# Kernel tuning notes

Hardware: AMD Instinct MI355X
Metric: run time of the kernel (lower is better)

Reference implementation:

```python
import jax, jax.numpy as jnp
import numpy as np
import math

B, S, D, H, FF = 8, 1024, 1024, 16, 4096
DH = D // H
EPS = 1e-5


def _layernorm(x, g, b):
    mu = jnp.mean(x, axis=-1, keepdims=True)
    var = jnp.mean((x - mu) ** 2, axis=-1, keepdims=True)
    return (x - mu) * jax.lax.rsqrt(var + EPS) * g + b


def _gelu_tanh(x):
    c = math.sqrt(2.0 / math.pi)
    return 0.5 * x * (1.0 + jnp.tanh(c * (x + 0.044715 * x ** 3)))


def setup_inputs() -> dict:
    key = jax.random.key(0)
    ks = jax.random.split(key, 8)
    s = lambda d: 1.0 / math.sqrt(d)
    return {
        "x": jax.random.normal(ks[0], (B, S, D), jnp.float32),
        "ln1_g": jnp.ones((D,), jnp.float32),
        "ln1_b": jnp.zeros((D,), jnp.float32),
        "w_qkv": jax.random.normal(ks[1], (3 * D, D), jnp.float32) * s(D),
        "b_qkv": jax.random.normal(ks[2], (3 * D,), jnp.float32) * 0.02,
        "w_o": jax.random.normal(ks[3], (D, D), jnp.float32) * s(D),
        "b_o": jax.random.normal(ks[4], (D,), jnp.float32) * 0.02,
        "ln2_g": jnp.ones((D,), jnp.float32),
        "ln2_b": jnp.zeros((D,), jnp.float32),
        "w1": jax.random.normal(ks[5], (FF, D), jnp.float32) * s(D),
        "b1": jax.random.normal(ks[6], (FF,), jnp.float32) * 0.02,
        "w2": jax.random.normal(ks[7], (D, FF), jnp.float32) * s(FF),
        "b2": jnp.zeros((D,), jnp.float32),
    }


def reference(x, ln1_g, ln1_b, w_qkv, b_qkv, w_o, b_o, ln2_g, ln2_b, w1, b1, w2, b2):
    # --- pre-LN causal self-attention ---
    h = _layernorm(x, ln1_g, ln1_b)
    qkv = h @ w_qkv.T + b_qkv                      # [B,S,3D]
    q, k, v = jnp.split(qkv, 3, axis=-1)
    q = q.reshape(B, S, H, DH)
    k = k.reshape(B, S, H, DH)
    v = v.reshape(B, S, H, DH)
    scores = jnp.einsum("bqhd,bkhd->bhqk", q, k) / math.sqrt(DH)
    causal = jnp.triu(jnp.ones((S, S), jnp.bool_), 1)  # True above diagonal
    scores = jnp.where(causal, -jnp.inf, scores)
    attn = jax.nn.softmax(scores, axis=-1)
    o = jnp.einsum("bhqk,bkhd->bqhd", attn, v).reshape(B, S, D)
    x = x + (o @ w_o.T + b_o)
    # --- FFN ---
    h = _layernorm(x, ln2_g, ln2_b)
    h = _gelu_tanh(h @ w1.T + b1) @ w2.T + b2
    return x + h
```

## Files before the change

### kernel.cpp

```cpp
#include <hip/hip_runtime.h>
#include <math.h>


typedef __bf16 bf16_t;
typedef __bf16 bf16x4 __attribute__((ext_vector_type(4)));
typedef __bf16 bf16x8 __attribute__((ext_vector_type(8)));
typedef float f32x4 __attribute__((ext_vector_type(4)));

__device__ __forceinline__ void async16(const void* g, void* l) {
    __builtin_amdgcn_global_load_lds(
        (const __attribute__((address_space(1))) void*)g,
        (__attribute__((address_space(3))) void*)l,
        16, 0, 0);
}

__global__ __launch_bounds__(256) void f2b_all(
    const float* __restrict__ s0, const float* __restrict__ s1,
    const float* __restrict__ s2, const float* __restrict__ s3,
    bf16_t* __restrict__ d0, bf16_t* __restrict__ d1,
    bf16_t* __restrict__ d2, bf16_t* __restrict__ d3) {
    const int g = blockIdx.x * 256 + threadIdx.x;
    const float* s;
    bf16_t* d;
    int off;
    if (g < 786432)       { s = s0; d = d0; off = g; }
    else if (g < 1048576) { s = s1; d = d1; off = g - 786432; }
    else if (g < 2097152) { s = s2; d = d2; off = g - 1048576; }
    else                  { s = s3; d = d3; off = g - 2097152; }
    const int i = off * 4;
    const float4 v = *(const float4*)(s + i);
    bf16x4 o;
    o[0] = (bf16_t)v.x; o[1] = (bf16_t)v.y; o[2] = (bf16_t)v.z; o[3] = (bf16_t)v.w;
    *(bf16x4*)(d + i) = o;
}

__global__ __launch_bounds__(256) void ln_bf16(const float* __restrict__ x,
                                               const float* __restrict__ g,
                                               const float* __restrict__ bb,
                                               bf16_t* __restrict__ out) {
    const int tid = threadIdx.x;
    const int row = blockIdx.x;
    const float4 xv = *(const float4*)(x + row * 1024 + tid * 4);
    float s1 = xv.x + xv.y + xv.z + xv.w;
    float s2 = xv.x * xv.x + xv.y * xv.y + xv.z * xv.z + xv.w * xv.w;
#pragma unroll
    for (int m = 32; m >= 1; m >>= 1) {
        s1 += __shfl_xor(s1, m);
        s2 += __shfl_xor(s2, m);
    }
    __shared__ float r1[4], r2[4];
    const int wid = tid >> 6, lane = tid & 63;
    if (lane == 0) { r1[wid] = s1; r2[wid] = s2; }
    __syncthreads();
    s1 = r1[0] + r1[1] + r1[2] + r1[3];
    s2 = r2[0] + r2[1] + r2[2] + r2[3];
    const float mu = s1 * (1.0f / 1024.0f);
    const float var = s2 * (1.0f / 1024.0f) - mu * mu;
    const float rs = rsqrtf(var + 1e-5f);
    const float4 gv = *(const float4*)(g + tid * 4);
    const float4 bv = *(const float4*)(bb + tid * 4);
    bf16x4 o;
    o[0] = (bf16_t)((xv.x - mu) * rs * gv.x + bv.x);
    o[1] = (bf16_t)((xv.y - mu) * rs * gv.y + bv.y);
    o[2] = (bf16_t)((xv.z - mu) * rs * gv.z + bv.z);
    o[3] = (bf16_t)((xv.w - mu) * rs * gv.w + bv.w);
    *(bf16x4*)(out + row * 1024 + tid * 4) = o;
}

template <int MODE>
__global__ __launch_bounds__(256, 2) void gemm_bt(
    const bf16_t* __restrict__ A, const bf16_t* __restrict__ W,
    const float* __restrict__ bias, const float* __restrict__ resid,
    bf16_t* __restrict__ outb, float* __restrict__ outf,
    bf16_t* __restrict__ vt, int N, int K) {
    __shared__ bf16_t As[128 * 64];
    __shared__ bf16_t Bs[128 * 64];
    const int tid = threadIdx.x;
    const int w = tid >> 6;
    const int lane = tid & 63;
    const int l15 = lane & 15;
    const int quad = lane >> 4;

    const int nbn = N >> 7;
    const int per = 8 * nbn;
    const int lid = blockIdx.x;
    const int bm = (lid / per) * 8 + (lid % per) % 8;
    const int bn = (lid % per) / 8;
    const int m0 = bm * 128;
    const int n0 = bn * 128;
    const int wm = (w & 1) * 64;
    const int wn = (w >> 1) * 64;

    int rr[4], so[4];
#pragma unroll
    for (int q = 0; q < 4; q++) {
        const int c = q * 256 + w * 64 + lane;
        rr[q] = c >> 3;
        so[q] = ((c & 7) ^ (rr[q] & 7)) * 8;
    }
    const bf16_t* pA[4];
    const bf16_t* pB[4];
#pragma unroll
    for (int q = 0; q < 4; q++) {
        pA[q] = A + (size_t)(m0 + rr[q]) * K + so[q];
        pB[q] = W + (size_t)(n0 + rr[q]) * K + so[q];
    }

    f32x4 acc[4][4] = {};

    for (int k0 = 0; k0 < K; k0 += 64) {
#pragma unroll
        for (int q = 0; q < 4; q++) {
            async16(pA[q], As + q * 2048 + w * 512);
            async16(pB[q], Bs + q * 2048 + w * 512);
            pA[q] += 64; pB[q] += 64;
        }
        __syncthreads();

        bf16x8 af[4][2], bfr[4][2];
#pragma unroll
        for (int i = 0; i < 4; i++) {
            const int r = wm + i * 16 + l15;
#pragma unroll
            for (int f = 0; f < 2; f++) {
                const int slot = (f * 4 + quad) ^ (r & 7);
                af[i][f] = *(const bf16x8*)(As + r * 64 + slot * 8);
            }
        }
#pragma unroll
        for (int j = 0; j < 4; j++) {
            const int r = wn + j * 16 + l15;
#pragma unroll
            for (int f = 0; f < 2; f++) {
                const int slot = (f * 4 + quad) ^ (r & 7);
                bfr[j][f] = *(const bf16x8*)(Bs + r * 64 + slot * 8);
            }
        }
#pragma unroll
        for (int i = 0; i < 4; i++)
#pragma unroll
            for (int j = 0; j < 4; j++)
#pragma unroll
                for (int f = 0; f < 2; f++)
                    acc[i][j] = __builtin_amdgcn_mfma_f32_16x16x32_bf16(
                        af[i][f], bfr[j][f], acc[i][j], 0, 0, 0);
        __syncthreads();
    }

#pragma unroll
    for (int i = 0; i < 4; i++) {
#pragma unroll
        for (int j = 0; j < 4; j++) {
            const int col = n0 + wn + j * 16 + l15;
            const float bcol = bias[col];
            const int row0 = m0 + wm + i * 16 + quad * 4;
            float v4[4];
#pragma unroll
            for (int q = 0; q < 4; q++) {
                float v = acc[i][j][q] + bcol;
                if (MODE == 1) {
                    const float u2 = -1.5957691216057308f * (v + 0.044715f * v * v * v);
                    v = v * __builtin_amdgcn_rcpf(1.0f + __expf(u2));
                }
                v4[q] = v;
            }
            if (MODE == 2) {
#pragma unroll
                for (int q = 0; q < 4; q++) {
                    const size_t idx = (size_t)(row0 + q) * N + col;
                    outf[idx] = v4[q] + resid[idx];
                }
            } else if (MODE == 3 && col >= 2048) {
                const int bh = (row0 >> 10) * 16 + ((col - 2048) >> 6);
                const int d = (col - 2048) & 63;
                bf16x4 pk;
#pragma unroll
                for (int q = 0; q < 4; q++) pk[q] = (bf16_t)v4[q];
                *(bf16x4*)(vt + (size_t)bh * 65536 + d * 1024 + (row0 & 1023)) = pk;
            } else {
#pragma unroll
                for (int q = 0; q < 4; q++)
                    outb[(size_t)(row0 + q) * N + col] = (bf16_t)v4[q];
            }
        }
    }
}

__global__ __launch_bounds__(256) void attn_mfma(const bf16_t* __restrict__ qkv,
                                                 const bf16_t* __restrict__ vt,
                                                 bf16_t* __restrict__ o) {
    __shared__ bf16_t Ks[4096];
    __shared__ bf16_t Vs[4096];
    __shared__ bf16_t Ps[4][16][72];
    const int tid = threadIdx.x;
    const int w = tid >> 6;
    const int lane = tid & 63;
    const int l15 = lane & 15;
    const int quad = lane >> 4;
    const int qb = blockIdx.x;
    const int bh = blockIdx.y;
    const int b = bh >> 4, h = bh & 15;

    const int qrow = b * 1024 + qb * 64 + w * 16;
    const int qmaxw = qb * 64 + w * 16 + 15;

    bf16x8 qf[2];
#pragma unroll
    for (int f = 0; f < 2; f++) {
        bf16x8 t = *(const bf16x8*)(qkv + (size_t)(qrow + l15) * 3072 + h * 64 + f * 32 + quad * 8);
#pragma unroll
        for (int e = 0; e < 8; e++) t[e] = (bf16_t)((float)t[e] * 0.125f);
        qf[f] = t;
    }

    f32x4 Ot[4] = {};
    float mrow = -3.0e38f, lrow = 0.0f;

    const int c0 = w * 64 + lane;
    const int c1 = 256 + c0;
    const int r0 = c0 >> 3, g0 = (((c0 & 7) ^ (r0 & 7))) * 8;
    const int r1 = c1 >> 3, g1 = (((c1 & 7) ^ (r1 & 7))) * 8;

    const bf16_t* kbase = qkv + (size_t)(b * 1024) * 3072 + 1024 + h * 64;
    const bf16_t* vbase = vt + (size_t)bh * 64 * 1024;

    for (int kt = 0; kt <= qb; kt++) {
        async16(kbase + (size_t)(kt * 64 + r0) * 3072 + g0, Ks + w * 512);
        async16(kbase + (size_t)(kt * 64 + r1) * 3072 + g1, Ks + 2048 + w * 512);
        async16(vbase + (size_t)r0 * 1024 + kt * 64 + g0, Vs + w * 512);
        async16(vbase + (size_t)r1 * 1024 + kt * 64 + g1, Vs + 2048 + w * 512);
        __syncthreads();

        f32x4 sf[4];
#pragma unroll
        for (int kb = 0; kb < 4; kb++) {
            if (kt * 64 + kb * 16 > qmaxw) {
                sf[kb] = (f32x4){-3.0e38f, -3.0e38f, -3.0e38f, -3.0e38f};
                continue;
            }
            const int r = kb * 16 + l15;
            f32x4 acc = {};
#pragma unroll
            for (int f = 0; f < 2; f++) {
                const int seg = (f * 4 + quad) ^ (r & 7);
                const bf16x8 kf = *(const bf16x8*)(Ks + r * 64 + seg * 8);
                acc = __builtin_amdgcn_mfma_f32_16x16x32_bf16(kf, qf[f], acc, 0, 0, 0);
            }
            if (kt == qb && kb == w) {
#pragma unroll
                for (int rr2 = 0; rr2 < 4; rr2++)
                    if (quad * 4 + rr2 > l15) acc[rr2] = -3.0e38f;
            }
            sf[kb] = acc;
        }

        float tmax = -3.0e38f;
#pragma unroll
        for (int kb = 0; kb < 4; kb++)
#pragma unroll
            for (int rr2 = 0; rr2 < 4; rr2++) tmax = fmaxf(tmax, sf[kb][rr2]);
        tmax = fmaxf(tmax, __shfl_xor(tmax, 16));
        tmax = fmaxf(tmax, __shfl_xor(tmax, 32));
        const float mnew = fmaxf(mrow, tmax);
        const float alpha = __expf(mrow - mnew);
        float psum = 0.0f;
#pragma unroll
        for (int kb = 0; kb < 4; kb++) {
            bf16x4 pk;
#pragma unroll
            for (int rr2 = 0; rr2 < 4; rr2++) {
                const float p = __expf(sf[kb][rr2] - mnew);
                psum += p;
                pk[rr2] = (bf16_t)p;
            }
            *(bf16x4*)(&Ps[w][l15][kb * 16 + quad * 4]) = pk;
        }
        psum += __shfl_xor(psum, 16);
        psum += __shfl_xor(psum, 32);
        lrow = lrow * alpha + psum;
        mrow = mnew;
#pragma unroll
        for (int db = 0; db < 4; db++)
#pragma unroll
            for (int rr2 = 0; rr2 < 4; rr2++) Ot[db][rr2] *= alpha;

#pragma unroll
        for (int ks = 0; ks < 2; ks++) {
            if (kt * 64 + ks * 32 > qmaxw) break;
            const bf16x8 pf = *(const bf16x8*)(&Ps[w][l15][ks * 32 + quad * 8]);
#pragma unroll
            for (int db = 0; db < 4; db++) {
                const int d = db * 16 + l15;
                const int seg = (ks * 4 + quad) ^ (d & 7);
                const bf16x8 vf = *(const bf16x8*)(Vs + d * 64 + seg * 8);
                Ot[db] = __builtin_amdgcn_mfma_f32_16x16x32_bf16(vf, pf, Ot[db], 0, 0, 0);
            }
        }
        __syncthreads();
    }

    const float rl = 1.0f / lrow;
#pragma unroll
    for (int db = 0; db < 4; db++) {
        bf16x4 ov;
#pragma unroll
        for (int rr2 = 0; rr2 < 4; rr2++) ov[rr2] = (bf16_t)(Ot[db][rr2] * rl);
        *(bf16x4*)(o + (size_t)(qrow + l15) * 1024 + h * 64 + db * 16 + quad * 4) = ov;
    }
}

extern "C" void kernel_launch(void* const* d_in, const int* in_sizes, int n_in,
                              void* d_out, int out_size, void* d_ws, size_t ws_size,
                              hipStream_t stream) {
    const float* x     = (const float*)d_in[0];
    const float* ln1g  = (const float*)d_in[1];
    const float* ln1b  = (const float*)d_in[2];
    const float* w_qkv = (const float*)d_in[3];
    const float* b_qkv = (const float*)d_in[4];
    const float* w_o   = (const float*)d_in[5];
    const float* b_o   = (const float*)d_in[6];
    const float* ln2g  = (const float*)d_in[7];
    const float* ln2b  = (const float*)d_in[8];
    const float* w1    = (const float*)d_in[9];
    const float* b1    = (const float*)d_in[10];
    const float* w2    = (const float*)d_in[11];
    const float* b2    = (const float*)d_in[12];
    float* out = (float*)d_out;

    char* w = (char*)d_ws;
    bf16_t* wbqkv = (bf16_t*)(w + 0);
    bf16_t* wbo   = (bf16_t*)(w + 6291456);
    bf16_t* wb1   = (bf16_t*)(w + 8388608);
    bf16_t* wb2   = (bf16_t*)(w + 16777216);
    bf16_t* h     = (bf16_t*)(w + 25165824);
    bf16_t* qkv   = (bf16_t*)(w + 41943040);
    bf16_t* ob    = (bf16_t*)(w + 92274688);
    float*  x1    = (float*)(w + 109051904);
    bf16_t* f     = (bf16_t*)(w + 142606336);
    bf16_t* vtb   = (bf16_t*)(w + 142606336);

    f2b_all<<<12288, 256, 0, stream>>>(w_qkv, w_o, w1, w2, wbqkv, wbo, wb1, wb2);

    ln_bf16<<<8192, 256, 0, stream>>>(x, ln1g, ln1b, h);
    gemm_bt<3><<<64 * 24, 256, 0, stream>>>(h, wbqkv, b_qkv, nullptr, qkv, nullptr, vtb, 3072, 1024);
    attn_mfma<<<dim3(16, 128), 256, 0, stream>>>(qkv, vtb, ob);
    gemm_bt<2><<<64 * 8, 256, 0, stream>>>(ob, wbo, b_o, x, nullptr, x1, nullptr, 1024, 1024);
    ln_bf16<<<8192, 256, 0, stream>>>(x1, ln2g, ln2b, h);
    gemm_bt<1><<<64 * 32, 256, 0, stream>>>(h, wb1, b1, nullptr, f, nullptr, nullptr, 4096, 1024);
    gemm_bt<2><<<64 * 8, 256, 0, stream>>>(f, wb2, b2, x1, nullptr, out, nullptr, 1024, 4096);
}
```

Before: 477.8 us.

## Widen attention query tile to 128 rows with 8 waves; fuse prep kernels

The attention kernel now processes 128 query rows per block using 512 threads (8 waves). Each 64-key K/V tile loaded into LDS is therefore shared by twice as many queries, which halves the global K/V traffic per query. The causal diagonal masking indices are adjusted to match. Separately, the weight fp32-to-bf16 conversion and the first layernorm are merged into one launch to save a kernel boundary. In exchange, the larger blocks make causal load balancing coarser and raise per-block LDS and register use, which can lower occupancy.

```diff
diff --git a/kernel.cpp b/kernel.cpp
--- a/kernel.cpp
+++ b/kernel.cpp
@@ -14,32 +14,11 @@
         16, 0, 0);
 }
 
-__global__ __launch_bounds__(256) void f2b_all(
-    const float* __restrict__ s0, const float* __restrict__ s1,
-    const float* __restrict__ s2, const float* __restrict__ s3,
-    bf16_t* __restrict__ d0, bf16_t* __restrict__ d1,
-    bf16_t* __restrict__ d2, bf16_t* __restrict__ d3) {
-    const int g = blockIdx.x * 256 + threadIdx.x;
-    const float* s;
-    bf16_t* d;
-    int off;
-    if (g < 786432)       { s = s0; d = d0; off = g; }
-    else if (g < 1048576) { s = s1; d = d1; off = g - 786432; }
-    else if (g < 2097152) { s = s2; d = d2; off = g - 1048576; }
-    else                  { s = s3; d = d3; off = g - 2097152; }
-    const int i = off * 4;
-    const float4 v = *(const float4*)(s + i);
-    bf16x4 o;
-    o[0] = (bf16_t)v.x; o[1] = (bf16_t)v.y; o[2] = (bf16_t)v.z; o[3] = (bf16_t)v.w;
-    *(bf16x4*)(d + i) = o;
-}
-
-__global__ __launch_bounds__(256) void ln_bf16(const float* __restrict__ x,
-                                               const float* __restrict__ g,
-                                               const float* __restrict__ bb,
-                                               bf16_t* __restrict__ out) {
+__device__ __forceinline__ void ln_row(const float* __restrict__ x,
+                                       const float* __restrict__ g,
+                                       const float* __restrict__ bb,
+                                       bf16_t* __restrict__ out, int row) {
     const int tid = threadIdx.x;
-    const int row = blockIdx.x;
     const float4 xv = *(const float4*)(x + row * 1024 + tid * 4);
     float s1 = xv.x + xv.y + xv.z + xv.w;
     float s2 = xv.x * xv.x + xv.y * xv.y + xv.z * xv.z + xv.w * xv.w;
@@ -67,6 +46,39 @@
     *(bf16x4*)(out + row * 1024 + tid * 4) = o;
 }
 
+__global__ __launch_bounds__(256) void prep(
+    const float* __restrict__ s0, const float* __restrict__ s1,
+    const float* __restrict__ s2, const float* __restrict__ s3,
+    bf16_t* __restrict__ d0, bf16_t* __restrict__ d1,
+    bf16_t* __restrict__ d2, bf16_t* __restrict__ d3,
+    const float* __restrict__ x, const float* __restrict__ ln1g,
+    const float* __restrict__ ln1b, bf16_t* __restrict__ h) {
+    if (blockIdx.x >= 12288) {
+        ln_row(x, ln1g, ln1b, h, blockIdx.x - 12288);
+        return;
+    }
+    const int g = blockIdx.x * 256 + threadIdx.x;
+    const float* s;
+    bf16_t* d;
+    int off;
+    if (g < 786432)       { s = s0; d = d0; off = g; }
+    else if (g < 1048576) { s = s1; d = d1; off = g - 786432; }
+    else if (g < 2097152) { s = s2; d = d2; off = g - 1048576; }
+    else                  { s = s3; d = d3; off = g - 2097152; }
+    const int i = off * 4;
+    const float4 v = *(const float4*)(s + i);
+    bf16x4 o;
+    o[0] = (bf16_t)v.x; o[1] = (bf16_t)v.y; o[2] = (bf16_t)v.z; o[3] = (bf16_t)v.w;
+    *(bf16x4*)(d + i) = o;
+}
+
+__global__ __launch_bounds__(256) void ln_bf16(const float* __restrict__ x,
+                                               const float* __restrict__ g,
+                                               const float* __restrict__ bb,
+                                               bf16_t* __restrict__ out) {
+    ln_row(x, g, bb, out, blockIdx.x);
+}
+
 template <int MODE>
 __global__ __launch_bounds__(256, 2) void gemm_bt(
     const bf16_t* __restrict__ A, const bf16_t* __restrict__ W,
@@ -186,12 +198,12 @@
     }
 }
 
-__global__ __launch_bounds__(256) void attn_mfma(const bf16_t* __restrict__ qkv,
+__global__ __launch_bounds__(512) void attn_mfma(const bf16_t* __restrict__ qkv,
                                                  const bf16_t* __restrict__ vt,
                                                  bf16_t* __restrict__ o) {
     __shared__ bf16_t Ks[4096];
     __shared__ bf16_t Vs[4096];
-    __shared__ bf16_t Ps[4][16][72];
+    __shared__ bf16_t Ps[8][16][72];
     const int tid = threadIdx.x;
     const int w = tid >> 6;
     const int lane = tid & 63;
@@ -201,8 +213,10 @@
     const int bh = blockIdx.y;
     const int b = bh >> 4, h = bh & 15;
 
-    const int qrow = b * 1024 + qb * 64 + w * 16;
-    const int qmaxw = qb * 64 + w * 16 + 15;
+    const int qrow = b * 1024 + qb * 128 + w * 16;
+    const int qmaxw = qb * 128 + w * 16 + 15;
+    const int ktd = qmaxw >> 6;
+    const int kbd = w & 3;
 
     bf16x8 qf[2];
 #pragma unroll
@@ -217,18 +231,15 @@
     float mrow = -3.0e38f, lrow = 0.0f;
 
     const int c0 = w * 64 + lane;
-    const int c1 = 256 + c0;
     const int r0 = c0 >> 3, g0 = (((c0 & 7) ^ (r0 & 7))) * 8;
-    const int r1 = c1 >> 3, g1 = (((c1 & 7) ^ (r1 & 7))) * 8;
 
     const bf16_t* kbase = qkv + (size_t)(b * 1024) * 3072 + 1024 + h * 64;
     const bf16_t* vbase = vt + (size_t)bh * 64 * 1024;
 
-    for (int kt = 0; kt <= qb; kt++) {
+    const int ktmax = 2 * qb + 1;
+    for (int kt = 0; kt <= ktmax; kt++) {
         async16(kbase + (size_t)(kt * 64 + r0) * 3072 + g0, Ks + w * 512);
-        async16(kbase + (size_t)(kt * 64 + r1) * 3072 + g1, Ks + 2048 + w * 512);
         async16(vbase + (size_t)r0 * 1024 + kt * 64 + g0, Vs + w * 512);
-        async16(vbase + (size_t)r1 * 1024 + kt * 64 + g1, Vs + 2048 + w * 512);
         __syncthreads();
 
         f32x4 sf[4];
@@ -246,7 +257,7 @@
                 const bf16x8 kf = *(const bf16x8*)(Ks + r * 64 + seg * 8);
                 acc = __builtin_amdgcn_mfma_f32_16x16x32_bf16(kf, qf[f], acc, 0, 0, 0);
             }
-            if (kt == qb && kb == w) {
+            if (kt == ktd && kb == kbd) {
 #pragma unroll
                 for (int rr2 = 0; rr2 < 4; rr2++)
                     if (quad * 4 + rr2 > l15) acc[rr2] = -3.0e38f;
@@ -339,11 +350,10 @@
     bf16_t* f     = (bf16_t*)(w + 142606336);
     bf16_t* vtb   = (bf16_t*)(w + 142606336);
 
-    f2b_all<<<12288, 256, 0, stream>>>(w_qkv, w_o, w1, w2, wbqkv, wbo, wb1, wb2);
-
-    ln_bf16<<<8192, 256, 0, stream>>>(x, ln1g, ln1b, h);
+    prep<<<20480, 256, 0, stream>>>(w_qkv, w_o, w1, w2, wbqkv, wbo, wb1, wb2,
+                                    x, ln1g, ln1b, h);
     gemm_bt<3><<<64 * 24, 256, 0, stream>>>(h, wbqkv, b_qkv, nullptr, qkv, nullptr, vtb, 3072, 1024);
-    attn_mfma<<<dim3(16, 128), 256, 0, stream>>>(qkv, vtb, ob);
+    attn_mfma<<<dim3(8, 128), 512, 0, stream>>>(qkv, vtb, ob);
     gemm_bt<2><<<64 * 8, 256, 0, stream>>>(ob, wbo, b_o, x, nullptr, x1, nullptr, 1024, 1024);
     ln_bf16<<<8192, 256, 0, stream>>>(x1, ln2g, ln2b, h);
     gemm_bt<1><<<64 * 32, 256, 0, stream>>>(h, wb1, b1, nullptr, f, nullptr, nullptr, 4096, 1024);
```

New measurement: 471.4 us. About the same (-1.3%).
